# Optimization experiments

Measured on AMD Instinct MI355X. Metric: run time of the kernel, lower is better.

## Reference

```python
import jax, jax.numpy as jnp
import numpy as np
import math

B, T, C, H = 4, 2048, 1024, 4
D = C // H
SCALE = 1.0 / math.sqrt(D)
EPS = 1e-5

def _cln(x, w, b):
    # channel-first LayerNorm over C of (B, C, T)
    mu = jnp.mean(x, axis=1, keepdims=True)
    r = x - mu
    s = jnp.mean(r * r, axis=1, keepdims=True)
    return r / jnp.sqrt(s + EPS) * w + b

def _dwconv(x, w, b=None):
    # depthwise conv1d: x (B, C, T), w (C, 1, 3), stride 1, pad 1
    y = jax.lax.conv_general_dilated(x, w, (1,), [(1, 1)], dimension_numbers=('NCH', 'OIH', 'NCH'), feature_group_count=x.shape[1])
    if b is not None:
        y = y + b[None, :, None]
    return y

def _conv1x1(x, w, b):
    # pointwise conv: x (B, C, T), w (Cout, Cin), b (Cout,)
    return jnp.einsum('oc,bct->bot', w, x) + b[None, :, None]

def _forward(x, mask, norm1_w, norm1_b, qconv_w, kconv_w, vconv_w, qnorm_w, qnorm_b, knorm_w, knorm_b, vnorm_w, vnorm_b, q1_w, q1_b, k1_w, k1_b, v1_w, v1_b, proj_w, proj_b, norm2_w, norm2_b, lin1_w, lin1_b, tc_w, tc_b, lin2_w, lin2_b):
    xc = jnp.swapaxes(x, 1, 2)                      # (B, C, T)
    h = _cln(xc, norm1_w, norm1_b)
    mf = mask.astype(x.dtype)                       # (B, 1, T); stride 1 -> interpolate is identity
    q = _conv1x1(_cln(_dwconv(h, qconv_w) * mf, qnorm_w, qnorm_b), q1_w, q1_b)
    k = _conv1x1(_cln(_dwconv(h, kconv_w) * mf, knorm_w, knorm_b), k1_w, k1_b)
    v = _conv1x1(_cln(_dwconv(h, vconv_w) * mf, vnorm_w, vnorm_b), v1_w, v1_b)
    # (B, H, T, D)
    q = jnp.swapaxes(q.reshape(B, H, D, T), 2, 3)
    k = jnp.swapaxes(k.reshape(B, H, D, T), 2, 3)
    v = jnp.swapaxes(v.reshape(B, H, D, T), 2, 3)
    att = jnp.einsum('bhqd,bhkd->bhqk', q * SCALE, k)
    att = jnp.where(mask[:, :, None, :], att, -jnp.inf)
    att = jax.nn.softmax(att, axis=-1)
    out = jnp.einsum('bhqk,bhkd->bhqd', att, v * mf[:, :, :, None])
    out = jnp.swapaxes(out, 2, 3).reshape(B, C, T)
    out = _conv1x1(out, proj_w, proj_b) * mf        # qx_mask == mask for stride 1
    x = x + jnp.swapaxes(out, 1, 2)                 # residual, (B, T, C)
    # Local_cnn branch
    h2 = jnp.swapaxes(_cln(jnp.swapaxes(x, 1, 2), norm2_w, norm2_b), 1, 2)  # (B, T, C)
    y = h2 @ lin1_w.T + lin1_b
    y = jnp.swapaxes(_dwconv(jnp.swapaxes(y, 1, 2), tc_w, tc_b), 1, 2)
    y = jax.nn.gelu(y, approximate=False)
    y = y @ lin2_w.T + lin2_b
    return x + y

def setup_inputs():
    key = jax.random.key(0)
    ks = jax.random.split(key, 16)
    f32 = jnp.float32
    x = jax.random.normal(ks[0], (B, T, C), dtype=f32)
    lengths = jax.random.randint(ks[1], (B,), T // 2, T + 1)
    mask = jnp.arange(T)[None, None, :] < lengths[:, None, None]  # (B, 1, T) bool
    dw_std = math.sqrt(2.0 / 3.0)
    px_std = math.sqrt(2.0 / C)
    d = dict(x=x, mask=mask)
    d['norm1_w'] = jnp.ones((1, C, 1), f32); d['norm1_b'] = jnp.zeros((1, C, 1), f32)
    d['qconv_w'] = jax.random.normal(ks[2], (C, 1, 3), dtype=f32) * dw_std
    d['kconv_w'] = jax.random.normal(ks[3], (C, 1, 3), dtype=f32) * dw_std
    d['vconv_w'] = jax.random.normal(ks[4], (C, 1, 3), dtype=f32) * dw_std
    for nm in ['qnorm', 'knorm', 'vnorm']:
        d[nm + '_w'] = jnp.ones((1, C, 1), f32); d[nm + '_b'] = jnp.zeros((1, C, 1), f32)
    d['q1_w'] = jax.random.normal(ks[5], (C, C), dtype=f32) * px_std; d['q1_b'] = jnp.zeros((C,), f32)
    d['k1_w'] = jax.random.normal(ks[6], (C, C), dtype=f32) * px_std; d['k1_b'] = jnp.zeros((C,), f32)
    d['v1_w'] = jax.random.normal(ks[7], (C, C), dtype=f32) * px_std; d['v1_b'] = jnp.zeros((C,), f32)
    d['proj_w'] = jax.random.normal(ks[8], (C, C), dtype=f32) * px_std; d['proj_b'] = jnp.zeros((C,), f32)
    d['norm2_w'] = jnp.ones((1, C, 1), f32); d['norm2_b'] = jnp.zeros((1, C, 1), f32)
    d['lin1_w'] = jax.random.normal(ks[9], (C, C), dtype=f32) * 0.02; d['lin1_b'] = jnp.zeros((C,), f32)
    d['tc_w'] = jax.random.normal(ks[10], (C, 1, 3), dtype=f32) * dw_std; d['tc_b'] = jnp.zeros((C,), f32)
    d['lin2_w'] = jax.random.normal(ks[11], (C, C), dtype=f32) * 0.02; d['lin2_b'] = jnp.zeros((C,), f32)
    return d

def reference(x, mask, norm1_w, norm1_b, qconv_w, kconv_w, vconv_w, qnorm_w, qnorm_b, knorm_w, knorm_b, vnorm_w, vnorm_b, q1_w, q1_b, k1_w, k1_b, v1_w, v1_b, proj_w, proj_b, norm2_w, norm2_b, lin1_w, lin1_b, tc_w, tc_b, lin2_w, lin2_b):
    return _forward(x, mask, norm1_w, norm1_b, qconv_w, kconv_w, vconv_w, qnorm_w, qnorm_b, knorm_w, knorm_b, vnorm_w, vnorm_b, q1_w, q1_b, k1_w, k1_b, v1_w, v1_b, proj_w, proj_b, norm2_w, norm2_b, lin1_w, lin1_b, tc_w, tc_b, lin2_w, lin2_b)
```

## Files before the change

kernel.cpp:

```cpp
#include <hip/hip_runtime.h>

#define BB 4
#define TT 2048
#define CC 1024
#define HH 4
#define DD 256
#define MM (BB*TT)

#define EPSV 1e-5f
#define NEGBIG (-1e30f)
#define SCALEV 0.0625f

typedef unsigned short u16;
typedef unsigned int   u32;
typedef __bf16 bf16x8 __attribute__((ext_vector_type(8)));
typedef float  f32x4  __attribute__((ext_vector_type(4)));

typedef u32 __attribute__((address_space(1))) gu32;
typedef u32 __attribute__((address_space(3))) lu32;

__device__ __forceinline__ u16 f2bf(float f){
  u32 u = __builtin_bit_cast(u32, f);
  u32 r = (u + 0x7fffu + ((u >> 16) & 1u)) >> 16;
  return (u16)r;
}
__device__ __forceinline__ float bf2f(u16 h){
  u32 u = ((u32)h) << 16;
  return __builtin_bit_cast(float, u);
}
__device__ __forceinline__ void gload_lds16(const u16* g, u16* l){
  __builtin_amdgcn_global_load_lds((const gu32*)g, (lu32*)l, 16, 0, 0);
}
__device__ __forceinline__ u32 cvtpk_bf16(float lo, float hi){
  u32 r;
  asm("v_cvt_pk_bf16_f32 %0, %1, %2" : "=v"(r) : "v"(lo), "v"(hi));
  return r;
}

__global__ __launch_bounds__(256) void conv_w_kernel(
    const float* __restrict__ w0, const float* __restrict__ w1, const float* __restrict__ w2,
    const float* __restrict__ w3, const float* __restrict__ w4, const float* __restrict__ w5,
    u16* __restrict__ o0, u16* __restrict__ o1, u16* __restrict__ o2,
    u16* __restrict__ o3, u16* __restrict__ o4, u16* __restrict__ o5){
  const int i = (blockIdx.x * 256 + threadIdx.x) * 4;
  const float* wsrc[6] = {w0,w1,w2,w3,w4,w5};
  u16* odst[6] = {o0,o1,o2,o3,o4,o5};
#pragma unroll
  for (int k = 0; k < 6; ++k){
    float4 v = *(const float4*)(wsrc[k] + i);
    ushort4 p; p.x=f2bf(v.x); p.y=f2bf(v.y); p.z=f2bf(v.z); p.w=f2bf(v.w);
    *(ushort4*)(odst[k] + i) = p;
  }
}

template<int OUTBF>
__global__ __launch_bounds__(256) void ln_rows(const float* __restrict__ x,
    const float* __restrict__ g, const float* __restrict__ be, void* __restrict__ out){
  const int row = blockIdx.x, tid = threadIdx.x;
  const float4 v = ((const float4*)(x + (size_t)row * CC))[tid];
  float s  = v.x + v.y + v.z + v.w;
  float ss = v.x*v.x + v.y*v.y + v.z*v.z + v.w*v.w;
  __shared__ float sb[8];
#pragma unroll
  for (int o = 1; o < 64; o <<= 1){ s += __shfl_xor(s, o); ss += __shfl_xor(ss, o); }
  const int wid = tid >> 6, lane = tid & 63;
  if (lane == 0){ sb[wid] = s; sb[4 + wid] = ss; }
  __syncthreads();
  s  = sb[0] + sb[1] + sb[2] + sb[3];
  ss = sb[4] + sb[5] + sb[6] + sb[7];
  const float mu = s * (1.0f / CC);
  const float rstd = rsqrtf(ss * (1.0f / CC) - mu * mu + EPSV);
  const float4 gg = ((const float4*)g)[tid];
  const float4 bb = ((const float4*)be)[tid];
  const float r0 = (v.x - mu) * rstd * gg.x + bb.x;
  const float r1 = (v.y - mu) * rstd * gg.y + bb.y;
  const float r2 = (v.z - mu) * rstd * gg.z + bb.z;
  const float r3 = (v.w - mu) * rstd * gg.w + bb.w;
  if (OUTBF){
    ushort4 p; p.x=f2bf(r0); p.y=f2bf(r1); p.z=f2bf(r2); p.w=f2bf(r3);
    *(ushort4*)((u16*)out + (size_t)row * CC + tid * 4) = p;
  } else {
    ((float4*)((float*)out + (size_t)row * CC))[tid] = make_float4(r0, r1, r2, r3);
  }
}

__global__ __launch_bounds__(256) void qkv_pre(const float* __restrict__ h,
    const int* __restrict__ mask,
    const float* __restrict__ qw, const float* __restrict__ kw, const float* __restrict__ vw,
    const float* __restrict__ qg, const float* __restrict__ qb2,
    const float* __restrict__ kg, const float* __restrict__ kb2,
    const float* __restrict__ vg, const float* __restrict__ vb2,
    u16* __restrict__ qn, u16* __restrict__ kn, u16* __restrict__ vn){
  const int row = blockIdx.x, tid = threadIdx.x;
  const int t = row & (TT - 1);
  const float mf = mask[row] ? 1.f : 0.f;
  const float4 z4 = make_float4(0.f, 0.f, 0.f, 0.f);
  const float4 x0 = ((const float4*)(h + (size_t)row * CC))[tid];
  const float4 xm = (t > 0)      ? ((const float4*)(h + (size_t)(row - 1) * CC))[tid] : z4;
  const float4 xp = (t < TT - 1) ? ((const float4*)(h + (size_t)(row + 1) * CC))[tid] : z4;
  const int c = tid * 4;
  const float am[4] = {xm.x, xm.y, xm.z, xm.w};
  const float a0[4] = {x0.x, x0.y, x0.z, x0.w};
  const float ap[4] = {xp.x, xp.y, xp.z, xp.w};
  float yq[4], yk[4], yv[4];
  float sq=0.f, ssq=0.f, sk=0.f, ssk=0.f, sv=0.f, ssv=0.f;
#pragma unroll
  for (int i = 0; i < 4; ++i){
    const float* qwp = qw + (c + i) * 3;
    const float* kwp = kw + (c + i) * 3;
    const float* vwp = vw + (c + i) * 3;
    const float q_ = (am[i]*qwp[0] + a0[i]*qwp[1] + ap[i]*qwp[2]) * mf;
    const float k_ = (am[i]*kwp[0] + a0[i]*kwp[1] + ap[i]*kwp[2]) * mf;
    const float v_ = (am[i]*vwp[0] + a0[i]*vwp[1] + ap[i]*vwp[2]) * mf;
    yq[i]=q_; yk[i]=k_; yv[i]=v_;
    sq+=q_; ssq+=q_*q_; sk+=k_; ssk+=k_*k_; sv+=v_; ssv+=v_*v_;
  }
  __shared__ float sb[24];
#pragma unroll
  for (int o = 1; o < 64; o <<= 1){
    sq += __shfl_xor(sq, o); ssq += __shfl_xor(ssq, o);
    sk += __shfl_xor(sk, o); ssk += __shfl_xor(ssk, o);
    sv += __shfl_xor(sv, o); ssv += __shfl_xor(ssv, o);
  }
  const int wid = tid >> 6, lane = tid & 63;
  if (lane == 0){
    sb[wid]=sq; sb[4+wid]=ssq; sb[8+wid]=sk; sb[12+wid]=ssk; sb[16+wid]=sv; sb[20+wid]=ssv;
  }
  __syncthreads();
  sq  = sb[0]+sb[1]+sb[2]+sb[3];    ssq = sb[4]+sb[5]+sb[6]+sb[7];
  sk  = sb[8]+sb[9]+sb[10]+sb[11];  ssk = sb[12]+sb[13]+sb[14]+sb[15];
  sv  = sb[16]+sb[17]+sb[18]+sb[19];ssv = sb[20]+sb[21]+sb[22]+sb[23];
  {
    const float mu = sq * (1.f/CC), rstd = rsqrtf(ssq*(1.f/CC) - mu*mu + EPSV);
    ushort4 p;
    p.x = f2bf((yq[0]-mu)*rstd*qg[c+0] + qb2[c+0]);
    p.y = f2bf((yq[1]-mu)*rstd*qg[c+1] + qb2[c+1]);
    p.z = f2bf((yq[2]-mu)*rstd*qg[c+2] + qb2[c+2]);
    p.w = f2bf((yq[3]-mu)*rstd*qg[c+3] + qb2[c+3]);
    *(ushort4*)(qn + (size_t)row * CC + c) = p;
  }
  {
    const float mu = sk * (1.f/CC), rstd = rsqrtf(ssk*(1.f/CC) - mu*mu + EPSV);
    ushort4 p;
    p.x = f2bf((yk[0]-mu)*rstd*kg[c+0] + kb2[c+0]);
    p.y = f2bf((yk[1]-mu)*rstd*kg[c+1] + kb2[c+1]);
    p.z = f2bf((yk[2]-mu)*rstd*kg[c+2] + kb2[c+2]);
    p.w = f2bf((yk[3]-mu)*rstd*kg[c+3] + kb2[c+3]);
    *(ushort4*)(kn + (size_t)row * CC + c) = p;
  }
  {
    const float mu = sv * (1.f/CC), rstd = rsqrtf(ssv*(1.f/CC) - mu*mu + EPSV);
    ushort4 p;
    p.x = f2bf((yv[0]-mu)*rstd*vg[c+0] + vb2[c+0]);
    p.y = f2bf((yv[1]-mu)*rstd*vg[c+1] + vb2[c+1]);
    p.z = f2bf((yv[2]-mu)*rstd*vg[c+2] + vb2[c+2]);
    p.w = f2bf((yv[3]-mu)*rstd*vg[c+3] + vb2[c+3]);
    *(ushort4*)(vn + (size_t)row * CC + c) = p;
  }
}

template<int MODE>
__global__ __launch_bounds__(256) void gemm_bt(
    const u16* __restrict__ A, const u16* __restrict__ Bw,
    const float* __restrict__ bias, void* __restrict__ out,
    const float* __restrict__ resid, const int* __restrict__ mask){
  __shared__ u16 As[128 * 32];
  __shared__ u16 Bs[128 * 32];
  const int tid = threadIdx.x, lane = tid & 63, wid = tid >> 6;
  const int wr = wid >> 1, wc = wid & 1;
  const int bm = blockIdx.x, bn = blockIdx.y;
  f32x4 acc[4][4];
#pragma unroll
  for (int i = 0; i < 4; ++i)
#pragma unroll
    for (int j = 0; j < 4; ++j) acc[i][j] = (f32x4){0.f, 0.f, 0.f, 0.f};
  const u16* gA = A  + (size_t)(bm * 128 + wid * 32 + (lane >> 2)) * CC + (lane & 3) * 8;
  const u16* gB = Bw + (size_t)(bn * 128 + wid * 32 + (lane >> 2)) * CC + (lane & 3) * 8;
  u16* lA = &As[wid * 1024];
  u16* lB = &Bs[wid * 1024];
  const int la = lane & 15, lg8 = (lane >> 4) * 8;
  for (int kt = 0; kt < CC / 32; ++kt){
    gload_lds16(gA + kt * 32, lA);
    gload_lds16(gA + kt * 32 + (size_t)16 * CC, lA + 512);
    gload_lds16(gB + kt * 32, lB);
    gload_lds16(gB + kt * 32 + (size_t)16 * CC, lB + 512);
    __syncthreads();
    bf16x8 af[4], bf[4];
#pragma unroll
    for (int mi = 0; mi < 4; ++mi) af[mi] = *(const bf16x8*)&As[(wr*64 + mi*16 + la)*32 + lg8];
#pragma unroll
    for (int ni = 0; ni < 4; ++ni) bf[ni] = *(const bf16x8*)&Bs[(wc*64 + ni*16 + la)*32 + lg8];
#pragma unroll
    for (int mi = 0; mi < 4; ++mi)
#pragma unroll
      for (int ni = 0; ni < 4; ++ni)
        acc[mi][ni] = __builtin_amdgcn_mfma_f32_16x16x32_bf16(af[mi], bf[ni], acc[mi][ni], 0, 0, 0);
    __syncthreads();
  }
  const int lg = lane >> 4;
#pragma unroll
  for (int mi = 0; mi < 4; ++mi){
    const int mb = bm * 128 + wr * 64 + mi * 16 + lg * 4;
#pragma unroll
    for (int ni = 0; ni < 4; ++ni){
      const int n = bn * 128 + wc * 64 + ni * 16 + la;
      const float bz = bias[n];
      if (MODE == 0){
        u16* o = (u16*)out;
#pragma unroll
        for (int j = 0; j < 4; ++j) o[(size_t)(mb + j) * CC + n] = f2bf(acc[mi][ni][j] + bz);
      } else if (MODE == 1){
        float* o = (float*)out;
#pragma unroll
        for (int j = 0; j < 4; ++j){
          const int m = mb + j;
          const float mf = mask[m] ? 1.f : 0.f;
          o[(size_t)m * CC + n] = (acc[mi][ni][j] + bz) * mf + resid[(size_t)m * CC + n];
        }
      } else if (MODE == 2){
        float* o = (float*)out;
#pragma unroll
        for (int j = 0; j < 4; ++j){
          const int m = mb + j;
          o[(size_t)m * CC + n] = acc[mi][ni][j] + bz + resid[(size_t)m * CC + n];
        }
      } else {
        u16* o = (u16*)out;
        const int bq = mb >> 11, tq = mb & (TT - 1);
        const int hq = n >> 8, dq = n & 255;
        ushort4 p;
        p.x = f2bf(acc[mi][ni][0] + bz); p.y = f2bf(acc[mi][ni][1] + bz);
        p.z = f2bf(acc[mi][ni][2] + bz); p.w = f2bf(acc[mi][ni][3] + bz);
        *(ushort4*)&o[(size_t)((bq * HH + hq) * DD + dq) * TT + tq] = p;
      }
    }
  }
}

__global__ __launch_bounds__(256, 3) void flash_attn(
    const u16* __restrict__ Q, const u16* __restrict__ Kg,
    const u16* __restrict__ Vt, const int* __restrict__ mask,
    u16* __restrict__ Oa){
  __shared__ __align__(16) u16 Ks[32 * 256];
  __shared__ __align__(16) u16 Vs[256 * 32];
  __shared__ __align__(16) u16 Ps[4][16 * 32];
  const int qt = blockIdx.x, bh = blockIdx.y;
  const int b = bh >> 2, h2 = bh & 3;
  const int tid = threadIdx.x, lane = tid & 63, wid = tid >> 6;
  const int la = lane & 15, lg = lane >> 4;

  const int* mrow = mask + b * TT;
  int len = 1024;
  {
    unsigned long long bal = __ballot(mrow[1024 + lane * 16] != 0);
    int ones = __popcll(bal);
    if (ones > 0){
      int lo = 1024 + (ones - 1) * 16;
      unsigned long long bal2 = __ballot(mrow[lo + la] != 0);
      len = lo + __popcll(bal2 & 0xFFFFull);
    }
  }
  const int nkt = (len + 31) >> 5;

  bf16x8 qf[8];
  const u16* qrow = Q + (size_t)(b * TT + qt * 64 + wid * 16 + la) * CC + h2 * DD + lg * 8;
#pragma unroll
  for (int kd = 0; kd < 8; ++kd) qf[kd] = *(const bf16x8*)(qrow + kd * 32);

  f32x4 oacc[16];
#pragma unroll
  for (int i = 0; i < 16; ++i) oacc[i] = (f32x4){0.f, 0.f, 0.f, 0.f};
  float mrun = NEGBIG, lrun = 0.f;

  const int krow = tid >> 5, kchk = tid & 31;
  const u16* ksrc = Kg + (size_t)(b * TT + krow) * CC + h2 * DD + (kchk ^ (krow & 7)) * 8;
  const int vrow = tid >> 2, vchk = tid & 3;
  const u16* vsrc = Vt + (size_t)(bh * DD + vrow) * TT + (vchk ^ (vrow & 3)) * 8;
  u16* kdst = (u16*)((char*)Ks + tid * 16);
  u16* vdst = (u16*)((char*)Vs + tid * 16);

#define STAGE_K(KT) { _Pragma("unroll") \
  for (int i = 0; i < 4; ++i) \
    gload_lds16(ksrc + (size_t)((KT) * 32 + i * 8) * CC, kdst + i * 2048); }
#define STAGE_V(KT) { _Pragma("unroll") \
  for (int i = 0; i < 4; ++i) \
    gload_lds16(vsrc + (size_t)(i * 64) * TT + (KT) * 32, vdst + i * 2048); }

  STAGE_K(0); STAGE_V(0);
  __syncthreads();

  const char* KsB = (const char*)Ks;
  const char* VsB = (const char*)Vs;
  char* PsB = (char*)&Ps[wid][0];
  const int swk = (la & 7) << 4;
  const int swq = (la & 3) << 4;
  const float sc2 = SCALEV * 1.44269504f;

  for (int kt = 0; kt < nkt; ++kt){
    f32x4 sfr[2];
#pragma unroll
    for (int fn = 0; fn < 2; ++fn){
      f32x4 s = (f32x4){0.f, 0.f, 0.f, 0.f};
      const int rk = fn * 16 + la;
#pragma unroll
      for (int kd = 0; kd < 8; ++kd){
        bf16x8 kf = *(const bf16x8*)(KsB + rk * 512 + ((kd * 64 + lg * 16) ^ swk));
        s = __builtin_amdgcn_mfma_f32_16x16x32_bf16(kf, qf[kd], s, 0, 0, 0);
      }
      sfr[fn] = s;
    }
    if (kt * 32 + 32 <= len){
      sfr[0] *= sc2; sfr[1] *= sc2;
    } else {
      const int kb = kt * 32 + lg * 4;
#pragma unroll
      for (int fn = 0; fn < 2; ++fn)
#pragma unroll
        for (int j = 0; j < 4; ++j)
          sfr[fn][j] = (kb + fn * 16 + j < len) ? sfr[fn][j] * sc2 : NEGBIG;
    }
    float tm = fmaxf(fmaxf(fmaxf(sfr[0][0], sfr[0][1]), fmaxf(sfr[0][2], sfr[0][3])),
                     fmaxf(fmaxf(sfr[1][0], sfr[1][1]), fmaxf(sfr[1][2], sfr[1][3])));
    tm = fmaxf(tm, __shfl_xor(tm, 16));
    tm = fmaxf(tm, __shfl_xor(tm, 32));
    if (!__all(tm <= mrun + 12.0f)){
      const float mn = fmaxf(mrun, tm);
      const float al = __builtin_exp2f(mrun - mn);
      mrun = mn; lrun *= al;
#pragma unroll
      for (int i = 0; i < 16; ++i) oacc[i] *= al;
    }
    float p0 = __builtin_exp2f(sfr[0][0] - mrun), p1 = __builtin_exp2f(sfr[0][1] - mrun);
    float p2 = __builtin_exp2f(sfr[0][2] - mrun), p3 = __builtin_exp2f(sfr[0][3] - mrun);
    float p4 = __builtin_exp2f(sfr[1][0] - mrun), p5 = __builtin_exp2f(sfr[1][1] - mrun);
    float p6 = __builtin_exp2f(sfr[1][2] - mrun), p7 = __builtin_exp2f(sfr[1][3] - mrun);
    float ts = ((p0 + p1) + (p2 + p3)) + ((p4 + p5) + (p6 + p7));
    ts += __shfl_xor(ts, 16);
    ts += __shfl_xor(ts, 32);
    lrun += ts;
    {
      uint2 w0; w0.x = cvtpk_bf16(p0, p1); w0.y = cvtpk_bf16(p2, p3);
      uint2 w1; w1.x = cvtpk_bf16(p4, p5); w1.y = cvtpk_bf16(p6, p7);
      *(uint2*)(PsB + la * 64 + ((lg * 8) ^ swq)) = w0;
      *(uint2*)(PsB + la * 64 + ((32 + lg * 8) ^ swq)) = w1;
    }
    __syncthreads();
    if (kt + 1 < nkt) STAGE_K(kt + 1);
    bf16x8 pf = *(const bf16x8*)(PsB + la * 64 + ((lg * 16) ^ swq));
#pragma unroll
    for (int mi = 0; mi < 16; ++mi){
      const int d = mi * 16 + la;
      bf16x8 vf = *(const bf16x8*)(VsB + d * 64 + ((lg * 16) ^ swq));
      oacc[mi] = __builtin_amdgcn_mfma_f32_16x16x32_bf16(vf, pf, oacc[mi], 0, 0, 0);
    }
    __syncthreads();
    if (kt + 1 < nkt) STAGE_V(kt + 1);
  }
  const float inv = 1.f / lrun;
  u16* orow = Oa + (size_t)(b * TT + qt * 64 + wid * 16 + la) * CC + h2 * DD + lg * 4;
#pragma unroll
  for (int mi = 0; mi < 16; ++mi){
    ushort4 p;
    p.x = f2bf(oacc[mi][0] * inv); p.y = f2bf(oacc[mi][1] * inv);
    p.z = f2bf(oacc[mi][2] * inv); p.w = f2bf(oacc[mi][3] * inv);
    *(ushort4*)(orow + mi * 16) = p;
  }
#undef STAGE_K
#undef STAGE_V
}

__global__ __launch_bounds__(256) void tc_gelu(const u16* __restrict__ y2,
    const float* __restrict__ w, const float* __restrict__ bias, u16* __restrict__ y3){
  const int row = blockIdx.x, tid = threadIdx.x;
  const int t = row & (TT - 1);
  const int c = tid * 4;
  ushort4 z4; z4.x = z4.y = z4.z = z4.w = 0;
  const ushort4 u0 = *(const ushort4*)(y2 + (size_t)row * CC + c);
  const ushort4 um = (t > 0)      ? *(const ushort4*)(y2 + (size_t)(row - 1) * CC + c) : z4;
  const ushort4 up = (t < TT - 1) ? *(const ushort4*)(y2 + (size_t)(row + 1) * CC + c) : z4;
  const float am[4] = {bf2f(um.x), bf2f(um.y), bf2f(um.z), bf2f(um.w)};
  const float a0[4] = {bf2f(u0.x), bf2f(u0.y), bf2f(u0.z), bf2f(u0.w)};
  const float ap[4] = {bf2f(up.x), bf2f(up.y), bf2f(up.z), bf2f(up.w)};
  u16 pv[4];
#pragma unroll
  for (int i = 0; i < 4; ++i){
    const float* wp = w + (c + i) * 3;
    const float yv = am[i] * wp[0] + a0[i] * wp[1] + ap[i] * wp[2] + bias[c + i];
    const float ge = 0.5f * yv * (1.f + erff(yv * 0.7071067811865475f));
    pv[i] = f2bf(ge);
  }
  ushort4 p; p.x = pv[0]; p.y = pv[1]; p.z = pv[2]; p.w = pv[3];
  *(ushort4*)(y3 + (size_t)row * CC + c) = p;
}

extern "C" void kernel_launch(void* const* d_in, const int* in_sizes, int n_in,
                              void* d_out, int out_size, void* d_ws, size_t ws_size,
                              hipStream_t stream){
  const float* x     = (const float*)d_in[0];
  const int*   mask  = (const int*)d_in[1];
  const float* n1g   = (const float*)d_in[2];
  const float* n1b   = (const float*)d_in[3];
  const float* qconv = (const float*)d_in[4];
  const float* kconv = (const float*)d_in[5];
  const float* vconv = (const float*)d_in[6];
  const float* qg    = (const float*)d_in[7];
  const float* qbe   = (const float*)d_in[8];
  const float* kg    = (const float*)d_in[9];
  const float* kbe   = (const float*)d_in[10];
  const float* vg    = (const float*)d_in[11];
  const float* vbe   = (const float*)d_in[12];
  const float* q1w   = (const float*)d_in[13];
  const float* q1b   = (const float*)d_in[14];
  const float* k1w   = (const float*)d_in[15];
  const float* k1b   = (const float*)d_in[16];
  const float* v1w   = (const float*)d_in[17];
  const float* v1b   = (const float*)d_in[18];
  const float* pw    = (const float*)d_in[19];
  const float* pb    = (const float*)d_in[20];
  const float* n2g   = (const float*)d_in[21];
  const float* n2b   = (const float*)d_in[22];
  const float* l1w   = (const float*)d_in[23];
  const float* l1b   = (const float*)d_in[24];
  const float* tcw   = (const float*)d_in[25];
  const float* tcb   = (const float*)d_in[26];
  const float* l2w   = (const float*)d_in[27];
  const float* l2b   = (const float*)d_in[28];
  (void)in_sizes; (void)n_in; (void)out_size; (void)ws_size;

  char* ws = (char*)d_ws;
  const size_t MB = (size_t)1 << 20;
  u16* wq  = (u16*)(ws + 0 * MB);
  u16* wk  = (u16*)(ws + 2 * MB);
  u16* wv  = (u16*)(ws + 4 * MB);
  u16* wp2 = (u16*)(ws + 6 * MB);
  u16* wl1 = (u16*)(ws + 8 * MB);
  u16* wl2 = (u16*)(ws + 10 * MB);
  float* hbuf = (float*)(ws + 12 * MB);
  float* x2   = hbuf;
  u16* qn  = (u16*)(ws + 44 * MB);
  u16* kn  = (u16*)(ws + 60 * MB);
  u16* vn  = (u16*)(ws + 76 * MB);
  u16* Qb  = (u16*)(ws + 92 * MB);
  u16* Kb  = (u16*)(ws + 108 * MB);
  u16* Vtb = (u16*)(ws + 124 * MB);
  u16* AO  = qn;
  u16* y1  = kn;
  u16* y2  = vn;
  u16* y3  = Qb;

  conv_w_kernel<<<1024, 256, 0, stream>>>(q1w, k1w, v1w, pw, l1w, l2w, wq, wk, wv, wp2, wl1, wl2);
  ln_rows<0><<<MM, 256, 0, stream>>>(x, n1g, n1b, hbuf);
  qkv_pre<<<MM, 256, 0, stream>>>(hbuf, mask, qconv, kconv, vconv,
                                  qg, qbe, kg, kbe, vg, vbe, qn, kn, vn);
  gemm_bt<0><<<dim3(64, 8), 256, 0, stream>>>(qn, wq, q1b, Qb, nullptr, nullptr);
  gemm_bt<0><<<dim3(64, 8), 256, 0, stream>>>(kn, wk, k1b, Kb, nullptr, nullptr);
  gemm_bt<3><<<dim3(64, 8), 256, 0, stream>>>(vn, wv, v1b, Vtb, nullptr, nullptr);
  flash_attn<<<dim3(32, 16), 256, 0, stream>>>(Qb, Kb, Vtb, mask, AO);
  gemm_bt<1><<<dim3(64, 8), 256, 0, stream>>>(AO, wp2, pb, x2, x, mask);
  ln_rows<1><<<MM, 256, 0, stream>>>(x2, n2g, n2b, y1);
  gemm_bt<0><<<dim3(64, 8), 256, 0, stream>>>(y1, wl1, l1b, y2, nullptr, nullptr);
  tc_gelu<<<MM, 256, 0, stream>>>(y2, tcw, tcb, y3);
  gemm_bt<2><<<dim3(64, 8), 256, 0, stream>>>(y3, wl2, l2b, (float*)d_out, x2, nullptr);
}
```

Baseline: 377.5 us.

## Double-buffer K/V tiles in flash attention and remap block order

The flash attention kernel now keeps two LDS buffers each for K and V. The next tile's loads are issued at the top of each iteration, which removes one of the two barriers per iteration. The V and P LDS layouts switch from an XOR swizzle to an 80-byte padded row stride, and the grid becomes 1D with a remap so consecutive blocks spread across batch/head pairs, likely for L2/XCD locality. This costs twice the LDS and lowers the occupancy hint from 3 to 2 blocks. The single remaining barrier relies on the async LDS loads landing before the next read.

After: 376.5 us. About the same (-0.3%).

```diff
diff --git a/kernel.cpp b/kernel.cpp
--- a/kernel.cpp
+++ b/kernel.cpp
@@ -237,14 +237,16 @@
   }
 }
 
-__global__ __launch_bounds__(256, 3) void flash_attn(
+__global__ __launch_bounds__(256, 2) void flash_attn(
     const u16* __restrict__ Q, const u16* __restrict__ Kg,
     const u16* __restrict__ Vt, const int* __restrict__ mask,
     u16* __restrict__ Oa){
-  __shared__ __align__(16) u16 Ks[32 * 256];
-  __shared__ __align__(16) u16 Vs[256 * 32];
-  __shared__ __align__(16) u16 Ps[4][16 * 32];
-  const int qt = blockIdx.x, bh = blockIdx.y;
+  __shared__ __align__(16) u16 Ks[2][32 * 256];
+  __shared__ __align__(16) u16 Vs[2][1280 * 8];
+  __shared__ __align__(16) u16 Ps[4][640];
+  const int Dn = blockIdx.x;
+  const int bh = (Dn & 7) * 2 + ((Dn >> 3) >> 5);
+  const int qt = (Dn >> 3) & 31;
   const int b = bh >> 2, h2 = bh & 3;
   const int tid = threadIdx.x, lane = tid & 63, wid = tid >> 6;
   const int la = lane & 15, lg = lane >> 4;
@@ -274,29 +276,38 @@
 
   const int krow = tid >> 5, kchk = tid & 31;
   const u16* ksrc = Kg + (size_t)(b * TT + krow) * CC + h2 * DD + (kchk ^ (krow & 7)) * 8;
-  const int vrow = tid >> 2, vchk = tid & 3;
-  const u16* vsrc = Vt + (size_t)(bh * DD + vrow) * TT + (vchk ^ (vrow & 3)) * 8;
-  u16* kdst = (u16*)((char*)Ks + tid * 16);
-  u16* vdst = (u16*)((char*)Vs + tid * 16);
-
-#define STAGE_K(KT) { _Pragma("unroll") \
-  for (int i = 0; i < 4; ++i) \
-    gload_lds16(ksrc + (size_t)((KT) * 32 + i * 8) * CC, kdst + i * 2048); }
-#define STAGE_V(KT) { _Pragma("unroll") \
-  for (int i = 0; i < 4; ++i) \
-    gload_lds16(vsrc + (size_t)(i * 64) * TT + (KT) * 32, vdst + i * 2048); }
-
-  STAGE_K(0); STAGE_V(0);
+  u16* KsW = &Ks[0][0];
+  u16* VsW = &Vs[0][0];
+
+  auto stageK = [&](int KT, int BUF){
+#pragma unroll
+    for (int i = 0; i < 4; ++i)
+      gload_lds16(ksrc + (size_t)(KT * 32 + i * 8) * CC,
+                  KsW + BUF * 8192 + i * 2048 + wid * 512);
+  };
+  auto stageV = [&](int KT, int BUF){
+#pragma unroll
+    for (int i = 0; i < 5; ++i){
+      const int g = i * 256 + tid;
+      const int dd = g / 5, cc = g % 5;
+      if (cc < 4)
+        gload_lds16(Vt + (size_t)(bh * DD + dd) * TT + KT * 32 + cc * 8,
+                    VsW + BUF * 10240 + i * 2048 + wid * 512);
+    }
+  };
+
+  stageK(0, 0); stageV(0, 0);
   __syncthreads();
 
-  const char* KsB = (const char*)Ks;
-  const char* VsB = (const char*)Vs;
   char* PsB = (char*)&Ps[wid][0];
   const int swk = (la & 7) << 4;
-  const int swq = (la & 3) << 4;
   const float sc2 = SCALEV * 1.44269504f;
 
   for (int kt = 0; kt < nkt; ++kt){
+    const int cur = kt & 1;
+    if (kt + 1 < nkt){ stageK(kt + 1, cur ^ 1); stageV(kt + 1, cur ^ 1); }
+    const char* KsB = (const char*)&Ks[cur][0];
+    const char* VsB = (const char*)&Vs[cur][0];
     f32x4 sfr[2];
 #pragma unroll
     for (int fn = 0; fn < 2; ++fn){
@@ -341,20 +352,16 @@
     {
       uint2 w0; w0.x = cvtpk_bf16(p0, p1); w0.y = cvtpk_bf16(p2, p3);
       uint2 w1; w1.x = cvtpk_bf16(p4, p5); w1.y = cvtpk_bf16(p6, p7);
-      *(uint2*)(PsB + la * 64 + ((lg * 8) ^ swq)) = w0;
-      *(uint2*)(PsB + la * 64 + ((32 + lg * 8) ^ swq)) = w1;
+      *(uint2*)(PsB + la * 80 + lg * 8) = w0;
+      *(uint2*)(PsB + la * 80 + 32 + lg * 8) = w1;
+    }
+    bf16x8 pf = *(const bf16x8*)(PsB + la * 80 + lg * 16);
+#pragma unroll
+    for (int mi = 0; mi < 16; ++mi){
+      bf16x8 vf = *(const bf16x8*)(VsB + (mi * 16 + la) * 80 + lg * 16);
+      oacc[mi] = __builtin_amdgcn_mfma_f32_16x16x32_bf16(vf, pf, oacc[mi], 0, 0, 0);
     }
     __syncthreads();
-    if (kt + 1 < nkt) STAGE_K(kt + 1);
-    bf16x8 pf = *(const bf16x8*)(PsB + la * 64 + ((lg * 16) ^ swq));
-#pragma unroll
-    for (int mi = 0; mi < 16; ++mi){
-      const int d = mi * 16 + la;
-      bf16x8 vf = *(const bf16x8*)(VsB + d * 64 + ((lg * 16) ^ swq));
-      oacc[mi] = __builtin_amdgcn_mfma_f32_16x16x32_bf16(vf, pf, oacc[mi], 0, 0, 0);
-    }
-    __syncthreads();
-    if (kt + 1 < nkt) STAGE_V(kt + 1);
   }
   const float inv = 1.f / lrun;
   u16* orow = Oa + (size_t)(b * TT + qt * 64 + wid * 16 + la) * CC + h2 * DD + lg * 4;
@@ -365,8 +372,6 @@
     p.z = f2bf(oacc[mi][2] * inv); p.w = f2bf(oacc[mi][3] * inv);
     *(ushort4*)(orow + mi * 16) = p;
   }
-#undef STAGE_K
-#undef STAGE_V
 }
 
 __global__ __launch_bounds__(256) void tc_gelu(const u16* __restrict__ y2,
@@ -455,7 +460,7 @@
   gemm_bt<0><<<dim3(64, 8), 256, 0, stream>>>(qn, wq, q1b, Qb, nullptr, nullptr);
   gemm_bt<0><<<dim3(64, 8), 256, 0, stream>>>(kn, wk, k1b, Kb, nullptr, nullptr);
   gemm_bt<3><<<dim3(64, 8), 256, 0, stream>>>(vn, wv, v1b, Vtb, nullptr, nullptr);
-  flash_attn<<<dim3(32, 16), 256, 0, stream>>>(Qb, Kb, Vtb, mask, AO);
+  flash_attn<<<512, 256, 0, stream>>>(Qb, Kb, Vtb, mask, AO);
   gemm_bt<1><<<dim3(64, 8), 256, 0, stream>>>(AO, wp2, pb, x2, x, mask);
   ln_rows<1><<<MM, 256, 0, stream>>>(x2, n2g, n2b, y1);
   gemm_bt<0><<<dim3(64, 8), 256, 0, stream>>>(y1, wl1, l1b, y2, nullptr, nullptr);
```
